# Optimization experiments

Hardware: AMD Instinct MI355X
Metric: run time of the kernel (lower is better)

## Reference

```python
import jax, jax.numpy as jnp
import numpy as np

H = 1024   # hidden_dim
B = 4096   # batch
T = 128    # forecast_len
IN = 1     # output_dim (univariate)


def setup_inputs() -> dict:
    key = jax.random.key(0)
    ks = jax.random.split(key, 8)
    s = 1.0 / np.sqrt(H)  # torch LSTM/Linear default uniform init scale
    u = lambda k, shape: jax.random.uniform(k, shape, jnp.float32, -s, s)
    return {
        "hidden": jax.random.normal(ks[0], (1, B, H), jnp.float32),
        "cell":   jax.random.normal(ks[1], (1, B, H), jnp.float32),
        "W_ih":   u(ks[2], (4 * H, IN)),   # torch gate order: i, f, g, o
        "W_hh":   u(ks[3], (4 * H, H)),
        "b_ih":   u(ks[4], (4 * H,)),
        "b_hh":   u(ks[5], (4 * H,)),
        "W_out":  u(ks[6], (IN, H)),
        "b_out":  u(ks[7], (IN,)),
    }


def reference(hidden, cell, W_ih, W_hh, b_ih, b_hh, W_out, b_out):
    h = hidden[0]  # [B, H]  (num_layers == 1)
    c = cell[0]    # [B, H]
    x0 = jnp.zeros((h.shape[0], IN), h.dtype)  # initial decoder input = zeros
    b = b_ih + b_hh

    def step(carry, _):
        x, h, c = carry
        gates = x @ W_ih.T + h @ W_hh.T + b          # [B, 4H]
        i, f, g, o = jnp.split(gates, 4, axis=-1)    # torch order i,f,g,o
        c = jax.nn.sigmoid(f) * c + jax.nn.sigmoid(i) * jnp.tanh(g)
        h = jax.nn.sigmoid(o) * jnp.tanh(c)
        pred = h @ W_out.T + b_out                   # [B, 1]
        return (pred, h, c), pred                    # prediction fed back as next input

    _, preds = jax.lax.scan(step, (x0, h, c), None, length=T)  # [T, B, 1]
    return jnp.transpose(preds, (1, 0, 2))  # [B, T, 1]
```

## Files before the change

### kernel.cpp

```cpp
#include <hip/hip_runtime.h>
#include <hip/hip_bf16.h>
#include <stdint.h>


#define HH 1024
#define BB 4096
#define TT 128

#define BM 128
#define BJ 32
#define BKK 64

typedef __bf16 bf16;
typedef __bf16 v8bf __attribute__((ext_vector_type(8)));
typedef float f32x4 __attribute__((ext_vector_type(4)));

__device__ __forceinline__ float fast_sigmoid(float x) {
    return 1.0f / (1.0f + __expf(-x));
}
__device__ __forceinline__ float fast_tanh(float x) {
    return 1.0f - 2.0f / (__expf(2.0f * x) + 1.0f);
}

__device__ __forceinline__ void gload_lds16(const void* g, void* l) {
    __builtin_amdgcn_global_load_lds(
        (const __attribute__((address_space(1))) uint32_t*)(uintptr_t)g,
        (__attribute__((address_space(3))) uint32_t*)(uint32_t)(uintptr_t)l,
        16, 0, 0);
}


__global__ void prep_weights(const float* __restrict__ Whh,
                             const float* __restrict__ bih,
                             const float* __restrict__ bhh,
                             bf16* __restrict__ Wr,
                             float* __restrict__ bias) {
    int idx = blockIdx.x * blockDim.x + threadIdx.x;
    if (idx < 4 * HH * HH) {
        int k   = idx & (HH - 1);
        int row = idx >> 10;
        int jb  = row >> 7;
        int g   = (row >> 5) & 3;
        int jj  = row & 31;
        int srow = g * HH + jb * 32 + jj;
        Wr[idx] = (bf16)Whh[srow * HH + k];
    }
    if (idx < 4 * HH) bias[idx] = bih[idx] + bhh[idx];
}

__global__ void prep_h(const float* __restrict__ h0, bf16* __restrict__ hb) {
    int idx = blockIdx.x * blockDim.x + threadIdx.x;
    if (idx < BB * HH) hb[idx] = (bf16)h0[idx];
}

__global__ void prep_pred(float* __restrict__ predbuf, const float* __restrict__ b_out) {
    int idx = blockIdx.x * blockDim.x + threadIdx.x;
    if (idx < (TT + 1) * BB) predbuf[idx] = (idx < BB) ? 0.0f : b_out[0];
}


__global__ __launch_bounds__(128, 2)
void lstm_step(const bf16* __restrict__ hread, bf16* __restrict__ hwrite,
               const float* __restrict__ cin, float* __restrict__ cout,
               const bf16* __restrict__ Wr, const float* __restrict__ bias,
               const float* __restrict__ Wih, const float* __restrict__ Wout,
               const float* __restrict__ predbuf_r, float* __restrict__ predbuf_w) {
    __shared__ bf16 As[BM][BKK];
    __shared__ bf16 Bs[BM][BKK];

    const int tid  = threadIdx.x;
    const int lane = tid & 63;
    const int w    = tid >> 6;
    const int quad = lane >> 4, l15 = lane & 15;

    const int bid    = blockIdx.x;
    const int jb     = (bid & 7) * 4 + ((bid >> 3) & 3);
    const int blockB = (bid >> 5) * BM;

    f32x4 acc[4][8];
#pragma unroll
    for (int mi = 0; mi < 4; mi++)
#pragma unroll
        for (int nt = 0; nt < 8; nt++) acc[mi][nt] = (f32x4){0.f, 0.f, 0.f, 0.f};

    const bf16* Asrc = hread + (size_t)blockB * HH;
    const bf16* Bsrc = Wr + (size_t)jb * 128 * HH;

    const int r8 = lane >> 3;
    const int gc = (lane & 7) ^ r8;
    const int swr = l15 & 7;

    for (int k0 = 0; k0 < HH; k0 += BKK) {
#pragma unroll
        for (int c2 = 0; c2 < 8; c2++) {
            const int rowb = w * 64 + c2 * 8;
            gload_lds16(Asrc + (size_t)(rowb + r8) * HH + k0 + gc * 8, &As[rowb][0]);
            gload_lds16(Bsrc + (size_t)(rowb + r8) * HH + k0 + gc * 8, &Bs[rowb][0]);
        }
        asm volatile("s_waitcnt vmcnt(0)" ::: "memory");
        __syncthreads();
#pragma unroll
        for (int kk = 0; kk < 2; kk++) {
            v8bf a[4], b[8];
            const int pch = ((kk * 4 + quad) ^ swr) * 8;
#pragma unroll
            for (int mi = 0; mi < 4; mi++)
                a[mi] = *(const v8bf*)&As[w * 64 + mi * 16 + l15][pch];
#pragma unroll
            for (int nt = 0; nt < 8; nt++)
                b[nt] = *(const v8bf*)&Bs[nt * 16 + l15][pch];
#pragma unroll
            for (int mi = 0; mi < 4; mi++)
#pragma unroll
                for (int nt = 0; nt < 8; nt++)
                    acc[mi][nt] = __builtin_amdgcn_mfma_f32_16x16x32_bf16(
                        a[mi], b[nt], acc[mi][nt], 0, 0, 0);
        }
        __syncthreads();
    }

    float wihv[2][4], bsvv[2][4], wov[2];
#pragma unroll
    for (int jh = 0; jh < 2; jh++) {
        const int j = jb * 32 + jh * 16 + l15;
#pragma unroll
        for (int g = 0; g < 4; g++) {
            wihv[jh][g] = Wih[g * HH + j];
            bsvv[jh][g] = bias[g * HH + j];
        }
        wov[jh] = Wout[j];
    }

#pragma unroll
    for (int mi = 0; mi < 4; mi++) {
#pragma unroll
        for (int r = 0; r < 4; r++) {
            const int b = blockB + w * 64 + mi * 16 + quad * 4 + r;
            const float x = predbuf_r[b];
            float pacc = 0.0f;
#pragma unroll
            for (int jh = 0; jh < 2; jh++) {
                const int j = jb * 32 + jh * 16 + l15;
                const float gi = acc[mi][0 + jh][r] + x * wihv[jh][0] + bsvv[jh][0];
                const float gf = acc[mi][2 + jh][r] + x * wihv[jh][1] + bsvv[jh][1];
                const float gg = acc[mi][4 + jh][r] + x * wihv[jh][2] + bsvv[jh][2];
                const float go = acc[mi][6 + jh][r] + x * wihv[jh][3] + bsvv[jh][3];
                const float cn = fast_sigmoid(gf) * cin[(size_t)b * HH + j]
                               + fast_sigmoid(gi) * fast_tanh(gg);
                cout[(size_t)b * HH + j] = cn;
                const float hn = fast_sigmoid(go) * fast_tanh(cn);
                hwrite[(size_t)b * HH + j] = (bf16)hn;
                pacc += hn * wov[jh];
            }
            pacc += __shfl_xor(pacc, 1);
            pacc += __shfl_xor(pacc, 2);
            pacc += __shfl_xor(pacc, 4);
            pacc += __shfl_xor(pacc, 8);
            if (l15 == 0) atomicAdd(&predbuf_w[b], pacc);
        }
    }
}


__global__ void write_out(const float* __restrict__ predbuf, float* __restrict__ out) {
    int idx = blockIdx.x * blockDim.x + threadIdx.x;
    if (idx < BB * TT) {
        int t = idx & (TT - 1);
        int b = idx >> 7;
        out[idx] = predbuf[(size_t)(t + 1) * BB + b];
    }
}


extern "C" void kernel_launch(void* const* d_in, const int* in_sizes, int n_in,
                              void* d_out, int out_size, void* d_ws, size_t ws_size,
                              hipStream_t stream) {
    const float* hidden = (const float*)d_in[0];
    const float* cell   = (const float*)d_in[1];
    const float* Wih    = (const float*)d_in[2];
    const float* Whh    = (const float*)d_in[3];
    const float* bih    = (const float*)d_in[4];
    const float* bhh    = (const float*)d_in[5];
    const float* Wout   = (const float*)d_in[6];
    const float* bout   = (const float*)d_in[7];
    float* out = (float*)d_out;

    char* ws = (char*)d_ws;
    bf16* Wr = (bf16*)ws;        ws += (size_t)4 * HH * HH * 2;
    bf16* hb0 = (bf16*)ws;       ws += (size_t)BB * HH * 2;
    bf16* hb1 = (bf16*)ws;       ws += (size_t)BB * HH * 2;
    float* cbuf = (float*)ws;    ws += (size_t)BB * HH * 4;
    float* bias = (float*)ws;    ws += (size_t)4 * HH * 4;
    float* predbuf = (float*)ws; ws += (size_t)(TT + 1) * BB * 4;

    prep_weights<<<(4 * HH * HH + 255) / 256, 256, 0, stream>>>(Whh, bih, bhh, Wr, bias);
    prep_h<<<(BB * HH + 255) / 256, 256, 0, stream>>>(hidden, hb0);
    prep_pred<<<((TT + 1) * BB + 255) / 256, 256, 0, stream>>>(predbuf, bout);

    bf16* hb[2] = {hb0, hb1};
    for (int t = 0; t < TT; t++) {
        const bf16* hr = hb[t & 1];
        bf16* hw = hb[(t + 1) & 1];
        const float* ci = (t == 0) ? cell : cbuf;
        lstm_step<<<(HH / BJ) * (BB / BM), 128, 0, stream>>>(
            hr, hw, ci, cbuf, Wr, bias, Wih, Wout,
            predbuf + (size_t)t * BB, predbuf + (size_t)(t + 1) * BB);
    }

    write_out<<<(BB * TT + 255) / 256, 256, 0, stream>>>(predbuf, out);
}
```

Baseline: 6.132 ms.

## Widen LSTM step block tile to 64 hidden units with four waves

Each block now covers 64 hidden units (256 gate rows) instead of 32, using 256 threads split into a 2x2 wave grid, and the weight reordering is changed to match. Each loaded tile of h now feeds twice as many gate columns, which halves how often h is re-read across blocks and halves the block count. The cost is a larger LDS footprint per block (48KB), which may lower occupancy, and fewer blocks (512) to spread across the CUs.

```diff
diff --git a/kernel.cpp b/kernel.cpp
--- a/kernel.cpp
+++ b/kernel.cpp
@@ -8,7 +8,6 @@
 #define TT 128
 
 #define BM 128
-#define BJ 32
 #define BKK 64
 
 typedef __bf16 bf16;
@@ -39,10 +38,10 @@
     if (idx < 4 * HH * HH) {
         int k   = idx & (HH - 1);
         int row = idx >> 10;
-        int jb  = row >> 7;
-        int g   = (row >> 5) & 3;
-        int jj  = row & 31;
-        int srow = g * HH + jb * 32 + jj;
+        int jb2 = row >> 8;
+        int g   = (row >> 6) & 3;
+        int jj  = row & 63;
+        int srow = g * HH + jb2 * 64 + jj;
         Wr[idx] = (bf16)Whh[srow * HH + k];
     }
     if (idx < 4 * HH) bias[idx] = bih[idx] + bhh[idx];
@@ -59,23 +58,24 @@
 }
 
 
-__global__ __launch_bounds__(128, 2)
+__global__ __launch_bounds__(256, 2)
 void lstm_step(const bf16* __restrict__ hread, bf16* __restrict__ hwrite,
                const float* __restrict__ cin, float* __restrict__ cout,
                const bf16* __restrict__ Wr, const float* __restrict__ bias,
                const float* __restrict__ Wih, const float* __restrict__ Wout,
                const float* __restrict__ predbuf_r, float* __restrict__ predbuf_w) {
     __shared__ bf16 As[BM][BKK];
-    __shared__ bf16 Bs[BM][BKK];
-
-    const int tid  = threadIdx.x;
-    const int lane = tid & 63;
-    const int w    = tid >> 6;
-    const int quad = lane >> 4, l15 = lane & 15;
+    __shared__ bf16 Bs[2 * BM][BKK];
+
+    const int tid   = threadIdx.x;
+    const int lane  = tid & 63;
+    const int w     = tid >> 6;
+    const int waveM = w >> 1, waveN = w & 1;
+    const int quad  = lane >> 4, l15 = lane & 15;
 
     const int bid    = blockIdx.x;
-    const int jb     = (bid & 7) * 4 + ((bid >> 3) & 3);
-    const int blockB = (bid >> 5) * BM;
+    const int jb2    = (bid & 7) * 2 + ((bid >> 3) & 1);
+    const int blockB = (bid >> 4) * BM;
 
     f32x4 acc[4][8];
 #pragma unroll
@@ -84,17 +84,21 @@
         for (int nt = 0; nt < 8; nt++) acc[mi][nt] = (f32x4){0.f, 0.f, 0.f, 0.f};
 
     const bf16* Asrc = hread + (size_t)blockB * HH;
-    const bf16* Bsrc = Wr + (size_t)jb * 128 * HH;
-
-    const int r8 = lane >> 3;
-    const int gc = (lane & 7) ^ r8;
+    const bf16* Bsrc = Wr + (size_t)jb2 * 256 * HH;
+
+    const int r8  = lane >> 3;
+    const int gc  = (lane & 7) ^ r8;
     const int swr = l15 & 7;
 
     for (int k0 = 0; k0 < HH; k0 += BKK) {
+#pragma unroll
+        for (int c2 = 0; c2 < 4; c2++) {
+            const int rowb = w * 32 + c2 * 8;
+            gload_lds16(Asrc + (size_t)(rowb + r8) * HH + k0 + gc * 8, &As[rowb][0]);
+        }
 #pragma unroll
         for (int c2 = 0; c2 < 8; c2++) {
             const int rowb = w * 64 + c2 * 8;
-            gload_lds16(Asrc + (size_t)(rowb + r8) * HH + k0 + gc * 8, &As[rowb][0]);
             gload_lds16(Bsrc + (size_t)(rowb + r8) * HH + k0 + gc * 8, &Bs[rowb][0]);
         }
         asm volatile("s_waitcnt vmcnt(0)" ::: "memory");
@@ -105,10 +109,13 @@
             const int pch = ((kk * 4 + quad) ^ swr) * 8;
 #pragma unroll
             for (int mi = 0; mi < 4; mi++)
-                a[mi] = *(const v8bf*)&As[w * 64 + mi * 16 + l15][pch];
-#pragma unroll
-            for (int nt = 0; nt < 8; nt++)
-                b[nt] = *(const v8bf*)&Bs[nt * 16 + l15][pch];
+                a[mi] = *(const v8bf*)&As[waveM * 64 + mi * 16 + l15][pch];
+#pragma unroll
+            for (int g = 0; g < 4; g++)
+#pragma unroll
+                for (int jh = 0; jh < 2; jh++)
+                    b[g * 2 + jh] =
+                        *(const v8bf*)&Bs[g * 64 + waveN * 32 + jh * 16 + l15][pch];
 #pragma unroll
             for (int mi = 0; mi < 4; mi++)
 #pragma unroll
@@ -122,7 +129,7 @@
     float wihv[2][4], bsvv[2][4], wov[2];
 #pragma unroll
     for (int jh = 0; jh < 2; jh++) {
-        const int j = jb * 32 + jh * 16 + l15;
+        const int j = jb2 * 64 + waveN * 32 + jh * 16 + l15;
 #pragma unroll
         for (int g = 0; g < 4; g++) {
             wihv[jh][g] = Wih[g * HH + j];
@@ -135,12 +142,12 @@
     for (int mi = 0; mi < 4; mi++) {
 #pragma unroll
         for (int r = 0; r < 4; r++) {
-            const int b = blockB + w * 64 + mi * 16 + quad * 4 + r;
+            const int b = blockB + waveM * 64 + mi * 16 + quad * 4 + r;
             const float x = predbuf_r[b];
             float pacc = 0.0f;
 #pragma unroll
             for (int jh = 0; jh < 2; jh++) {
-                const int j = jb * 32 + jh * 16 + l15;
+                const int j = jb2 * 64 + waveN * 32 + jh * 16 + l15;
                 const float gi = acc[mi][0 + jh][r] + x * wihv[jh][0] + bsvv[jh][0];
                 const float gf = acc[mi][2 + jh][r] + x * wihv[jh][1] + bsvv[jh][1];
                 const float gg = acc[mi][4 + jh][r] + x * wihv[jh][2] + bsvv[jh][2];
@@ -202,7 +209,7 @@
         const bf16* hr = hb[t & 1];
         bf16* hw = hb[(t + 1) & 1];
         const float* ci = (t == 0) ? cell : cbuf;
-        lstm_step<<<(HH / BJ) * (BB / BM), 128, 0, stream>>>(
+        lstm_step<<<16 * (BB / BM), 256, 0, stream>>>(
             hr, hw, ci, cbuf, Wr, bias, Wih, Wout,
             predbuf + (size_t)t * BB, predbuf + (size_t)(t + 1) * BB);
     }
```

Measured after the change: 5.597 ms. -8.7%, faster.
